# Kernel tuning notes

Measured on AMD Instinct MI355X. Metric: run time of the kernel, lower is better.

## Reference

```python
import jax, jax.numpy as jnp
import numpy as np

N = 100000   # nodes
E = 1600000  # directed edges
NF = 128     # n_feat
NH = 128     # n_hid
NC = 64      # n_class


def _glorot(key, fan_in, fan_out):
    lim = (6.0 / (fan_in + fan_out)) ** 0.5
    return jax.random.uniform(key, (fan_in, fan_out), dtype=jnp.float32, minval=-lim, maxval=lim)


def setup_inputs() -> dict:
    key = jax.random.key(0)
    ks = jax.random.split(key, 10)
    x = jax.random.normal(ks[0], (N, NF), dtype=jnp.float32)
    edge_index = jax.random.randint(ks[1], (2, E), 0, N, dtype=jnp.int32)
    return {
        "x": x,
        "edge_index": edge_index,
        "W_in": _glorot(ks[2], NF, NH),
        "b_in": jnp.zeros((NH,), jnp.float32),
        "W_mid0": _glorot(ks[3], NH, NH),
        "b_mid0": jnp.zeros((NH,), jnp.float32),
        "W_mid1": _glorot(ks[4], NH, NH),
        "b_mid1": jnp.zeros((NH,), jnp.float32),
        "W_out": _glorot(ks[5], NH, NC),
        "b_out": jnp.zeros((NC,), jnp.float32),
        "W_skip_out": _glorot(ks[6], NH, NC),
    }


def _gcn_conv(x, W, b, src, dst, coef, n):
    # x' = D^-1/2 (A + I) D^-1/2 (x W) + b   (symmetric-normalized GCN conv)
    h = x @ W                               # [N, out]
    msg = h[src] * coef[:, None]            # [E+N, out] gather + scale
    return jax.ops.segment_sum(msg, dst, num_segments=n) + b


def reference(x, edge_index, W_in, b_in, W_mid0, b_mid0, W_mid1, b_mid1, W_out, b_out, W_skip_out):
    loops = jnp.arange(N, dtype=edge_index.dtype)
    src = jnp.concatenate([edge_index[0], loops])  # add self-loops
    dst = jnp.concatenate([edge_index[1], loops])
    deg = jax.ops.segment_sum(jnp.ones_like(dst, dtype=jnp.float32), dst, num_segments=N)
    dinv = jax.lax.rsqrt(deg)                      # deg >= 1 due to self-loops
    coef = dinv[src] * dinv[dst]                   # [E+N]

    # in layer: conv + res skip (NF == NH so plain add) + relu; dropout is no-op in eval
    h = _gcn_conv(x, W_in, b_in, src, dst, coef, N)
    x = jax.nn.relu(h + x)
    # mid layers
    for W, b in ((W_mid0, b_mid0), (W_mid1, b_mid1)):
        h = _gcn_conv(x, W, b, src, dst, coef, N)
        x = jax.nn.relu(h + x)
    # out layer: conv + res skip with channel projection NH -> NC
    h = _gcn_conv(x, W_out, b_out, src, dst, coef, N)
    return h + x @ W_skip_out
```

## Files before the change

kernel.cpp:

```cpp
#include <hip/hip_runtime.h>
#include <hip/hip_bf16.h>

constexpr int NN = 100000;
constexpr int NE = 1600000;
constexpr int NH = 128;
constexpr int NC = 64;
constexpr int BKN  = 256;
constexpr int NB2  = (NN + BKN - 1) / BKN;
constexpr int TILE = 4096;
constexpr int NT   = (NE + TILE - 1) / TILE;

__device__ __forceinline__ unsigned short f2bf(float f) {
    unsigned int u = __float_as_uint(f);
    unsigned int r = (u + 0x7fffu + ((u >> 16) & 1u)) >> 16;
    return (unsigned short)r;
}
__device__ __forceinline__ float bflo(unsigned int u) { return __uint_as_float(u << 16); }
__device__ __forceinline__ float bfhi(unsigned int u) { return __uint_as_float(u & 0xffff0000u); }
__device__ __forceinline__ float bf2f(unsigned short h) { return __uint_as_float(((unsigned int)h) << 16); }
__device__ __forceinline__ unsigned int pack2bf(float lo, float hi) {
    return (unsigned int)f2bf(lo) | ((unsigned int)f2bf(hi) << 16);
}

typedef __bf16 v8bf __attribute__((ext_vector_type(8)));
typedef float  v4f  __attribute__((ext_vector_type(4)));

constexpr size_t OFF_BCNT  = 0;
constexpr size_t OFF_BBASE = OFF_BCNT  + 2048;
constexpr size_t OFF_BCUR  = OFF_BBASE + 2048;
constexpr size_t OFF_RP    = OFF_BCUR  + 2048;
constexpr size_t OFF_DINV  = OFF_RP    + 400384;
constexpr size_t OFF_COL   = OFF_DINV  + 400384;
constexpr size_t OFF_WT    = OFF_COL   + 6400000;
constexpr size_t OFF_H     = OFF_WT    + 32768;
constexpr size_t OFF_X     = OFF_H     + 25600000;


__global__ __launch_bounds__(256) void bhist_kernel(const int* __restrict__ edst,
                                                    int* __restrict__ bcnt) {
    __shared__ int h[NB2];
    for (int i = threadIdx.x; i < NB2; i += 256) h[i] = 0;
    __syncthreads();
    const int base = blockIdx.x * TILE;
    #pragma unroll
    for (int j = 0; j < 16; ++j) {
        int e = base + j * 256 + threadIdx.x;
        if (e < NE) atomicAdd(&h[edst[e] >> 8], 1);
    }
    __syncthreads();
    for (int i = threadIdx.x; i < NB2; i += 256)
        if (h[i]) atomicAdd(&bcnt[i], h[i]);
}

__global__ __launch_bounds__(512) void bscan_kernel(const int* __restrict__ bcnt,
                                                    int* __restrict__ bbase,
                                                    int* __restrict__ bcur) {
    __shared__ int s[512];
    const int t = threadIdx.x;
    int v = (t < NB2) ? bcnt[t] : 0;
    s[t] = v;
    __syncthreads();
    for (int off = 1; off < 512; off <<= 1) {
        int a = (t >= off) ? s[t - off] : 0;
        __syncthreads();
        s[t] += a;
        __syncthreads();
    }
    int excl = s[t] - v;
    if (t < NB2) { bbase[t] = excl; bcur[t] = excl; }
    if (t == NB2 - 1) bbase[NB2] = excl + v;
}

__global__ __launch_bounds__(256) void scatter2_kernel(const int* __restrict__ esrc,
                                                       const int* __restrict__ edst,
                                                       int* __restrict__ bcur,
                                                       int2* __restrict__ ebuf) {
    __shared__ int h[NB2];
    __shared__ int cur[NB2];
    for (int i = threadIdx.x; i < NB2; i += 256) h[i] = 0;
    __syncthreads();
    const int base = blockIdx.x * TILE;
    #pragma unroll
    for (int j = 0; j < 16; ++j) {
        int e = base + j * 256 + threadIdx.x;
        if (e < NE) atomicAdd(&h[edst[e] >> 8], 1);
    }
    __syncthreads();
    for (int i = threadIdx.x; i < NB2; i += 256) {
        int c = h[i];
        cur[i] = c ? atomicAdd(&bcur[i], c) : 0;
    }
    __syncthreads();
    #pragma unroll
    for (int j = 0; j < 16; ++j) {
        int e = base + j * 256 + threadIdx.x;
        if (e < NE) {
            int s = esrc[e], d = edst[e];
            int pos = atomicAdd(&cur[d >> 8], 1);
            ebuf[pos] = make_int2(s, d);
        }
    }
}

__global__ __launch_bounds__(256) void csrfill2_kernel(const int2* __restrict__ ebuf,
                                                       const int* __restrict__ bbase,
                                                       int* __restrict__ rp,
                                                       float* __restrict__ dinv,
                                                       int* __restrict__ col) {
    __shared__ int cnt[256];
    __shared__ int cursor[256];
    __shared__ int s[256];
    __shared__ int sbeg, send;
    const int b = blockIdx.x;
    const int t = threadIdx.x;
    if (t == 0) { sbeg = bbase[b]; send = bbase[b + 1]; }
    cnt[t] = 0;
    __syncthreads();
    const int beg = sbeg, end = send;
    const int node0 = b * BKN;

    for (int e = beg + t; e < end; e += 256)
        atomicAdd(&cnt[ebuf[e].y & 255], 1);
    __syncthreads();

    int v = cnt[t];
    s[t] = v;
    __syncthreads();
    for (int off = 1; off < 256; off <<= 1) {
        int a = (t >= off) ? s[t - off] : 0;
        __syncthreads();
        s[t] += a;
        __syncthreads();
    }
    int excl = s[t] - v;
    int gnode = node0 + t;
    if (gnode < NN) {
        rp[gnode]   = beg + excl;
        dinv[gnode] = rsqrtf((float)(v + 1));
    }
    cursor[t] = beg + excl;
    if (b == NB2 - 1 && t == 0) rp[NN] = NE;
    __syncthreads();

    for (int e = beg + t; e < end; e += 256) {
        int2 sd = ebuf[e];
        int pos = atomicAdd(&cursor[sd.y & 255], 1);
        col[pos] = sd.x;
    }
}

__global__ __launch_bounds__(256) void wpre_kernel(const float* __restrict__ W0,
                                                   const float* __restrict__ W1,
                                                   int wstride,
                                                   unsigned short* __restrict__ Wt) {
    int e = blockIdx.x * 256 + threadIdx.x;
    int k = e >> 7, c = e & 127;
    float v = (c < 64) ? W0[(size_t)k * wstride + c] : W1[(size_t)k * wstride + (c - 64)];
    Wt[c * 128 + k] = f2bf(v);
}

constexpr int XROW = 136;

template<bool XF32>
__global__ __launch_bounds__(256) void gemm_mfma_kernel(const void* __restrict__ Xv,
                                                        const unsigned short* __restrict__ Wt,
                                                        const float* __restrict__ dinv,
                                                        int scaleMask,
                                                        unsigned short* __restrict__ Hb) {
    __shared__ unsigned short Wl[128 * XROW];
    __shared__ unsigned short Xl[64 * XROW];

    const int t = threadIdx.x;
    const int rowBase = blockIdx.x * 64;

    #pragma unroll
    for (int i = 0; i < 8; ++i) {
        int f = i * 256 + t;
        int r = f >> 4, c8 = f & 15;
        uint4 w = *(const uint4*)&Wt[r * 128 + c8 * 8];
        *(uint4*)&Wl[r * XROW + c8 * 8] = w;
    }
    if (XF32) {
        const float* X = (const float*)Xv;
        #pragma unroll
        for (int i = 0; i < 8; ++i) {
            int f = i * 256 + t;
            int r = f >> 5, c4 = f & 31;
            int gn = rowBase + r;
            float4 v = make_float4(0.f, 0.f, 0.f, 0.f);
            if (gn < NN) v = *(const float4*)&X[(size_t)gn * 128 + c4 * 4];
            ushort4 o;
            o.x = f2bf(v.x); o.y = f2bf(v.y); o.z = f2bf(v.z); o.w = f2bf(v.w);
            *(ushort4*)&Xl[r * XROW + c4 * 4] = o;
        }
    } else {
        const unsigned short* X = (const unsigned short*)Xv;
        #pragma unroll
        for (int i = 0; i < 4; ++i) {
            int f = i * 256 + t;
            int r = f >> 4, c8 = f & 15;
            int gn = rowBase + r;
            uint4 v = make_uint4(0u, 0u, 0u, 0u);
            if (gn < NN) v = *(const uint4*)&X[(size_t)gn * 128 + c8 * 8];
            *(uint4*)&Xl[r * XROW + c8 * 8] = v;
        }
    }
    __syncthreads();

    const int w  = t >> 6;
    const int l  = t & 63;
    const int lr = l & 15;
    const int lk = (l >> 4) * 8;

    v4f acc[8];
    #pragma unroll
    for (int n = 0; n < 8; ++n) acc[n] = (v4f){0.f, 0.f, 0.f, 0.f};

    const unsigned short* ax = &Xl[(w * 16 + lr) * XROW + lk];
    const unsigned short* bx = &Wl[lr * XROW + lk];

    #pragma unroll
    for (int kk = 0; kk < 4; ++kk) {
        v8bf a = *(const v8bf*)&ax[kk * 32];
        #pragma unroll
        for (int n = 0; n < 8; ++n) {
            v8bf b = *(const v8bf*)&bx[(n * 16) * XROW + kk * 32];
            acc[n] = __builtin_amdgcn_mfma_f32_16x16x32_bf16(a, b, acc[n], 0, 0, 0);
        }
    }

    #pragma unroll
    for (int r_ = 0; r_ < 4; ++r_) {
        int row  = w * 16 + (l >> 4) * 4 + r_;
        int grow = rowBase + row;
        float dsc = dinv[grow < NN ? grow : NN - 1];
        #pragma unroll
        for (int n = 0; n < 8; ++n) {
            float sc = ((scaleMask >> (n >> 2)) & 1) ? dsc : 1.f;
            Xl[row * XROW + n * 16 + lr] = f2bf(acc[n][r_] * sc);
        }
    }
    __syncthreads();

    #pragma unroll
    for (int i = 0; i < 4; ++i) {
        int f = i * 256 + t;
        int r = f >> 4, c8 = f & 15;
        int gn = rowBase + r;
        if (gn < NN) {
            uint4 v = *(const uint4*)&Xl[r * XROW + c8 * 8];
            *(uint4*)&Hb[(size_t)gn * 128 + c8 * 8] = v;
        }
    }
}

template<bool XF32>
__global__ __launch_bounds__(256) void agg128_kernel(const unsigned short* __restrict__ Hb,
                                                     const void* __restrict__ Xoldv,
                                                     const int* __restrict__ rp,
                                                     const int* __restrict__ col,
                                                     const float* __restrict__ dinv,
                                                     const float* __restrict__ bias,
                                                     unsigned int* __restrict__ Xnew) {
    const int wid  = threadIdx.x >> 6;
    const int lane = threadIdx.x & 63;
    const int i = blockIdx.x * 4 + wid;
    if (i >= NN) return;

    const unsigned int* __restrict__ Hu = (const unsigned int*)Hb;

    const float di = dinv[i];
    const float2 b2 = ((const float2*)bias)[lane];
    float xox, xoy;
    if (XF32) {
        float2 xo = ((const float2*)Xoldv)[(size_t)i * 64 + lane];
        xox = xo.x; xoy = xo.y;
    } else {
        unsigned int xo = ((const unsigned int*)Xoldv)[(size_t)i * 64 + lane];
        xox = bflo(xo); xoy = bfhi(xo);
    }

    unsigned int us = Hu[(size_t)i * 64 + lane];
    float ax = bflo(us), ay = bfhi(us);

    const int beg = rp[i], end = rp[i + 1];
    int e = beg;
    for (; e + 8 <= end; e += 8) {
        int s0 = col[e],     s1 = col[e + 1], s2 = col[e + 2], s3 = col[e + 3];
        int s4 = col[e + 4], s5 = col[e + 5], s6 = col[e + 6], s7 = col[e + 7];
        unsigned int u0 = Hu[(size_t)s0 * 64 + lane];
        unsigned int u1 = Hu[(size_t)s1 * 64 + lane];
        unsigned int u2 = Hu[(size_t)s2 * 64 + lane];
        unsigned int u3 = Hu[(size_t)s3 * 64 + lane];
        unsigned int u4 = Hu[(size_t)s4 * 64 + lane];
        unsigned int u5 = Hu[(size_t)s5 * 64 + lane];
        unsigned int u6 = Hu[(size_t)s6 * 64 + lane];
        unsigned int u7 = Hu[(size_t)s7 * 64 + lane];
        ax += ((bflo(u0) + bflo(u1)) + (bflo(u2) + bflo(u3))) +
              ((bflo(u4) + bflo(u5)) + (bflo(u6) + bflo(u7)));
        ay += ((bfhi(u0) + bfhi(u1)) + (bfhi(u2) + bfhi(u3))) +
              ((bfhi(u4) + bfhi(u5)) + (bfhi(u6) + bfhi(u7)));
    }
    for (; e + 4 <= end; e += 4) {
        int s0 = col[e], s1 = col[e + 1], s2 = col[e + 2], s3 = col[e + 3];
        unsigned int u0 = Hu[(size_t)s0 * 64 + lane];
        unsigned int u1 = Hu[(size_t)s1 * 64 + lane];
        unsigned int u2 = Hu[(size_t)s2 * 64 + lane];
        unsigned int u3 = Hu[(size_t)s3 * 64 + lane];
        ax += (bflo(u0) + bflo(u1)) + (bflo(u2) + bflo(u3));
        ay += (bfhi(u0) + bfhi(u1)) + (bfhi(u2) + bfhi(u3));
    }
    for (; e < end; ++e) {
        unsigned int u = Hu[(size_t)col[e] * 64 + lane];
        ax += bflo(u);
        ay += bfhi(u);
    }

    float ox = fmaxf(di * ax + b2.x + xox, 0.f);
    float oy = fmaxf(di * ay + b2.y + xoy, 0.f);
    Xnew[(size_t)i * 64 + lane] = pack2bf(ox, oy);
}

__global__ __launch_bounds__(256) void aggout_kernel(const unsigned short* __restrict__ Hb,
                                                     const int* __restrict__ rp,
                                                     const int* __restrict__ col,
                                                     const float* __restrict__ dinv,
                                                     const float* __restrict__ bias,
                                                     float* __restrict__ out) {
    const int wid  = threadIdx.x >> 6;
    const int lane = threadIdx.x & 63;
    const int i = blockIdx.x * 4 + wid;
    if (i >= NN) return;

    const float di = dinv[i];
    const float b  = bias[lane];
    const float sk = bf2f(Hb[(size_t)i * 128 + 64 + lane]);

    float a = bf2f(Hb[(size_t)i * 128 + lane]);
    const int beg = rp[i], end = rp[i + 1];
    int e = beg;
    for (; e + 8 <= end; e += 8) {
        int s0 = col[e],     s1 = col[e + 1], s2 = col[e + 2], s3 = col[e + 3];
        int s4 = col[e + 4], s5 = col[e + 5], s6 = col[e + 6], s7 = col[e + 7];
        float m0 = bf2f(Hb[(size_t)s0 * 128 + lane]);
        float m1 = bf2f(Hb[(size_t)s1 * 128 + lane]);
        float m2 = bf2f(Hb[(size_t)s2 * 128 + lane]);
        float m3 = bf2f(Hb[(size_t)s3 * 128 + lane]);
        float m4 = bf2f(Hb[(size_t)s4 * 128 + lane]);
        float m5 = bf2f(Hb[(size_t)s5 * 128 + lane]);
        float m6 = bf2f(Hb[(size_t)s6 * 128 + lane]);
        float m7 = bf2f(Hb[(size_t)s7 * 128 + lane]);
        a += ((m0 + m1) + (m2 + m3)) + ((m4 + m5) + (m6 + m7));
    }
    for (; e + 4 <= end; e += 4) {
        int s0 = col[e], s1 = col[e + 1], s2 = col[e + 2], s3 = col[e + 3];
        float m0 = bf2f(Hb[(size_t)s0 * 128 + lane]);
        float m1 = bf2f(Hb[(size_t)s1 * 128 + lane]);
        float m2 = bf2f(Hb[(size_t)s2 * 128 + lane]);
        float m3 = bf2f(Hb[(size_t)s3 * 128 + lane]);
        a += (m0 + m1) + (m2 + m3);
    }
    for (; e < end; ++e) a += bf2f(Hb[(size_t)col[e] * 128 + lane]);

    out[(size_t)i * 64 + lane] = di * a + b + sk;
}

extern "C" void kernel_launch(void* const* d_in, const int* in_sizes, int n_in,
                              void* d_out, int out_size, void* d_ws, size_t ws_size,
                              hipStream_t stream) {
    const float* x      = (const float*)d_in[0];
    const int*   ei     = (const int*)d_in[1];
    const float* W_in   = (const float*)d_in[2];
    const float* b_in   = (const float*)d_in[3];
    const float* W_mid0 = (const float*)d_in[4];
    const float* b_mid0 = (const float*)d_in[5];
    const float* W_mid1 = (const float*)d_in[6];
    const float* b_mid1 = (const float*)d_in[7];
    const float* W_out  = (const float*)d_in[8];
    const float* b_out  = (const float*)d_in[9];
    const float* W_skip = (const float*)d_in[10];

    const int* esrc = ei;
    const int* edst = ei + NE;

    char* ws = (char*)d_ws;
    int*   bcnt   = (int*)  (ws + OFF_BCNT);
    int*   bbase  = (int*)  (ws + OFF_BBASE);
    int*   bcur   = (int*)  (ws + OFF_BCUR);
    int*   rp     = (int*)  (ws + OFF_RP);
    float* dinv   = (float*)(ws + OFF_DINV);
    int*   col    = (int*)  (ws + OFF_COL);
    unsigned short* wt   = (unsigned short*)(ws + OFF_WT);
    unsigned short* hbuf = (unsigned short*)(ws + OFF_H);
    int2*  ebuf   = (int2*) (ws + OFF_H);
    unsigned short* xbuf = (unsigned short*)(ws + OFF_X);
    unsigned int*   xbufw = (unsigned int*)(ws + OFF_X);
    float* outp   = (float*)d_out;

    const int gemmGrid = (NN + 63) / 64;
    const int aggGrid  = (NN + 3) / 4;

    hipMemsetAsync(bcnt, 0, (size_t)(NB2 + 1) * 4, stream);
    bhist_kernel<<<NT, 256, 0, stream>>>(edst, bcnt);
    bscan_kernel<<<1, 512, 0, stream>>>(bcnt, bbase, bcur);
    scatter2_kernel<<<NT, 256, 0, stream>>>(esrc, edst, bcur, ebuf);
    csrfill2_kernel<<<NB2, 256, 0, stream>>>(ebuf, bbase, rp, dinv, col);

    wpre_kernel<<<64, 256, 0, stream>>>(W_in, W_in + 64, 128, wt);
    gemm_mfma_kernel<true><<<gemmGrid, 256, 0, stream>>>(x, wt, dinv, 3, hbuf);
    agg128_kernel<true><<<aggGrid, 256, 0, stream>>>(hbuf, x, rp, col, dinv, b_in, xbufw);

    wpre_kernel<<<64, 256, 0, stream>>>(W_mid0, W_mid0 + 64, 128, wt);
    gemm_mfma_kernel<false><<<gemmGrid, 256, 0, stream>>>(xbuf, wt, dinv, 3, hbuf);
    agg128_kernel<false><<<aggGrid, 256, 0, stream>>>(hbuf, xbuf, rp, col, dinv, b_mid0, xbufw);

    wpre_kernel<<<64, 256, 0, stream>>>(W_mid1, W_mid1 + 64, 128, wt);
    gemm_mfma_kernel<false><<<gemmGrid, 256, 0, stream>>>(xbuf, wt, dinv, 3, hbuf);
    agg128_kernel<false><<<aggGrid, 256, 0, stream>>>(hbuf, xbuf, rp, col, dinv, b_mid1, xbufw);

    wpre_kernel<<<64, 256, 0, stream>>>(W_out, W_skip, 64, wt);
    gemm_mfma_kernel<false><<<gemmGrid, 256, 0, stream>>>(xbuf, wt, dinv, 1, hbuf);
    aggout_kernel<<<aggGrid, 256, 0, stream>>>(hbuf, rp, col, dinv, b_out, outp);
}
```

Before: 385.9 us.

## Store hidden-layer gather features as FP8 and pack edge buffer into 32-bit words

The GEMM for the first three layers now writes the dinv-scaled hidden features as FP8 (e4m3) instead of bf16, and the aggregation kernels gather 2-byte FP8 pairs and convert them with the hardware packed converter. This halves the bytes fetched per neighbour in the random-gather aggregation, which is meant to be memory-bound. Separately, the CSR build packs source id and low destination byte into one 32-bit word instead of an int2, halving the temporary edge buffer traffic. The cost is a large precision loss in the hidden features, which may break accuracy tolerances. The packing also assumes node ids fit in 24 bits.

```diff
diff --git a/kernel.cpp b/kernel.cpp
--- a/kernel.cpp
+++ b/kernel.cpp
@@ -3,8 +3,6 @@
 
 constexpr int NN = 100000;
 constexpr int NE = 1600000;
-constexpr int NH = 128;
-constexpr int NC = 64;
 constexpr int BKN  = 256;
 constexpr int NB2  = (NN + BKN - 1) / BKN;
 constexpr int TILE = 4096;
@@ -24,6 +22,11 @@
 
 typedef __bf16 v8bf __attribute__((ext_vector_type(8)));
 typedef float  v4f  __attribute__((ext_vector_type(4)));
+typedef float  v2f  __attribute__((ext_vector_type(2)));
+
+__device__ __forceinline__ v2f fp8x2_to_f32(unsigned int u) {
+    return __builtin_amdgcn_cvt_pk_f32_fp8(u, false);
+}
 
 constexpr size_t OFF_BCNT  = 0;
 constexpr size_t OFF_BBASE = OFF_BCNT  + 2048;
@@ -32,7 +35,8 @@
 constexpr size_t OFF_DINV  = OFF_RP    + 400384;
 constexpr size_t OFF_COL   = OFF_DINV  + 400384;
 constexpr size_t OFF_WT    = OFF_COL   + 6400000;
-constexpr size_t OFF_H     = OFF_WT    + 32768;
+constexpr size_t OFF_H8    = OFF_WT    + 32768;
+constexpr size_t OFF_H     = OFF_H8    + 12800000;
 constexpr size_t OFF_X     = OFF_H     + 25600000;
 
 
@@ -74,7 +78,7 @@
 __global__ __launch_bounds__(256) void scatter2_kernel(const int* __restrict__ esrc,
                                                        const int* __restrict__ edst,
                                                        int* __restrict__ bcur,
-                                                       int2* __restrict__ ebuf) {
+                                                       unsigned int* __restrict__ ebuf) {
     __shared__ int h[NB2];
     __shared__ int cur[NB2];
     for (int i = threadIdx.x; i < NB2; i += 256) h[i] = 0;
@@ -97,12 +101,12 @@
         if (e < NE) {
             int s = esrc[e], d = edst[e];
             int pos = atomicAdd(&cur[d >> 8], 1);
-            ebuf[pos] = make_int2(s, d);
-        }
-    }
-}
-
-__global__ __launch_bounds__(256) void csrfill2_kernel(const int2* __restrict__ ebuf,
+            ebuf[pos] = (unsigned int)s | ((unsigned int)(d & 255) << 24);
+        }
+    }
+}
+
+__global__ __launch_bounds__(256) void csrfill2_kernel(const unsigned int* __restrict__ ebuf,
                                                        const int* __restrict__ bbase,
                                                        int* __restrict__ rp,
                                                        float* __restrict__ dinv,
@@ -120,7 +124,7 @@
     const int node0 = b * BKN;
 
     for (int e = beg + t; e < end; e += 256)
-        atomicAdd(&cnt[ebuf[e].y & 255], 1);
+        atomicAdd(&cnt[ebuf[e] >> 24], 1);
     __syncthreads();
 
     int v = cnt[t];
@@ -143,9 +147,9 @@
     __syncthreads();
 
     for (int e = beg + t; e < end; e += 256) {
-        int2 sd = ebuf[e];
-        int pos = atomicAdd(&cursor[sd.y & 255], 1);
-        col[pos] = sd.x;
+        unsigned int sd = ebuf[e];
+        int pos = atomicAdd(&cursor[sd >> 24], 1);
+        col[pos] = (int)(sd & 0xFFFFFFu);
     }
 }
 
@@ -161,12 +165,12 @@
 
 constexpr int XROW = 136;
 
-template<bool XF32>
+template<bool XF32, bool OUT8>
 __global__ __launch_bounds__(256) void gemm_mfma_kernel(const void* __restrict__ Xv,
                                                         const unsigned short* __restrict__ Wt,
                                                         const float* __restrict__ dinv,
                                                         int scaleMask,
-                                                        unsigned short* __restrict__ Hb) {
+                                                        void* __restrict__ Ho) {
     __shared__ unsigned short Wl[128 * XROW];
     __shared__ unsigned short Xl[64 * XROW];
 
@@ -242,20 +246,39 @@
     }
     __syncthreads();
 
-    #pragma unroll
-    for (int i = 0; i < 4; ++i) {
-        int f = i * 256 + t;
-        int r = f >> 4, c8 = f & 15;
-        int gn = rowBase + r;
-        if (gn < NN) {
-            uint4 v = *(const uint4*)&Xl[r * XROW + c8 * 8];
-            *(uint4*)&Hb[(size_t)gn * 128 + c8 * 8] = v;
+    if (OUT8) {
+        unsigned char* H8 = (unsigned char*)Ho;
+        #pragma unroll
+        for (int i = 0; i < 4; ++i) {
+            int f = i * 256 + t;
+            int r = f >> 4, c8 = f & 15;
+            int gn = rowBase + r;
+            if (gn < NN) {
+                uint4 v = *(const uint4*)&Xl[r * XROW + c8 * 8];
+                unsigned int lo = __builtin_amdgcn_cvt_pk_fp8_f32(bflo(v.x), bfhi(v.x), 0u, false);
+                lo = __builtin_amdgcn_cvt_pk_fp8_f32(bflo(v.y), bfhi(v.y), lo, true);
+                unsigned int hi = __builtin_amdgcn_cvt_pk_fp8_f32(bflo(v.z), bfhi(v.z), 0u, false);
+                hi = __builtin_amdgcn_cvt_pk_fp8_f32(bflo(v.w), bfhi(v.w), hi, true);
+                *(uint2*)&H8[(size_t)gn * 128 + c8 * 8] = make_uint2(lo, hi);
+            }
+        }
+    } else {
+        unsigned short* Hb = (unsigned short*)Ho;
+        #pragma unroll
+        for (int i = 0; i < 4; ++i) {
+            int f = i * 256 + t;
+            int r = f >> 4, c8 = f & 15;
+            int gn = rowBase + r;
+            if (gn < NN) {
+                uint4 v = *(const uint4*)&Xl[r * XROW + c8 * 8];
+                *(uint4*)&Hb[(size_t)gn * 128 + c8 * 8] = v;
+            }
         }
     }
 }
 
 template<bool XF32>
-__global__ __launch_bounds__(256) void agg128_kernel(const unsigned short* __restrict__ Hb,
+__global__ __launch_bounds__(256) void agg128_kernel(const unsigned char* __restrict__ H8,
                                                      const void* __restrict__ Xoldv,
                                                      const int* __restrict__ rp,
                                                      const int* __restrict__ col,
@@ -267,7 +290,7 @@
     const int i = blockIdx.x * 4 + wid;
     if (i >= NN) return;
 
-    const unsigned int* __restrict__ Hu = (const unsigned int*)Hb;
+    const unsigned short* __restrict__ Hs = (const unsigned short*)H8;
 
     const float di = dinv[i];
     const float2 b2 = ((const float2*)bias)[lane];
@@ -280,40 +303,44 @@
         xox = bflo(xo); xoy = bfhi(xo);
     }
 
-    unsigned int us = Hu[(size_t)i * 64 + lane];
-    float ax = bflo(us), ay = bfhi(us);
+    v2f sf = fp8x2_to_f32(Hs[(size_t)i * 64 + lane]);
+    float ax = sf.x, ay = sf.y;
 
     const int beg = rp[i], end = rp[i + 1];
     int e = beg;
     for (; e + 8 <= end; e += 8) {
         int s0 = col[e],     s1 = col[e + 1], s2 = col[e + 2], s3 = col[e + 3];
         int s4 = col[e + 4], s5 = col[e + 5], s6 = col[e + 6], s7 = col[e + 7];
-        unsigned int u0 = Hu[(size_t)s0 * 64 + lane];
-        unsigned int u1 = Hu[(size_t)s1 * 64 + lane];
-        unsigned int u2 = Hu[(size_t)s2 * 64 + lane];
-        unsigned int u3 = Hu[(size_t)s3 * 64 + lane];
-        unsigned int u4 = Hu[(size_t)s4 * 64 + lane];
-        unsigned int u5 = Hu[(size_t)s5 * 64 + lane];
-        unsigned int u6 = Hu[(size_t)s6 * 64 + lane];
-        unsigned int u7 = Hu[(size_t)s7 * 64 + lane];
-        ax += ((bflo(u0) + bflo(u1)) + (bflo(u2) + bflo(u3))) +
-              ((bflo(u4) + bflo(u5)) + (bflo(u6) + bflo(u7)));
-        ay += ((bfhi(u0) + bfhi(u1)) + (bfhi(u2) + bfhi(u3))) +
-              ((bfhi(u4) + bfhi(u5)) + (bfhi(u6) + bfhi(u7)));
+        unsigned int u0 = Hs[(size_t)s0 * 64 + lane];
+        unsigned int u1 = Hs[(size_t)s1 * 64 + lane];
+        unsigned int u2 = Hs[(size_t)s2 * 64 + lane];
+        unsigned int u3 = Hs[(size_t)s3 * 64 + lane];
+        unsigned int u4 = Hs[(size_t)s4 * 64 + lane];
+        unsigned int u5 = Hs[(size_t)s5 * 64 + lane];
+        unsigned int u6 = Hs[(size_t)s6 * 64 + lane];
+        unsigned int u7 = Hs[(size_t)s7 * 64 + lane];
+        v2f m0 = fp8x2_to_f32(u0), m1 = fp8x2_to_f32(u1);
+        v2f m2 = fp8x2_to_f32(u2), m3 = fp8x2_to_f32(u3);
+        v2f m4 = fp8x2_to_f32(u4), m5 = fp8x2_to_f32(u5);
+        v2f m6 = fp8x2_to_f32(u6), m7 = fp8x2_to_f32(u7);
+        ax += ((m0.x + m1.x) + (m2.x + m3.x)) + ((m4.x + m5.x) + (m6.x + m7.x));
+        ay += ((m0.y + m1.y) + (m2.y + m3.y)) + ((m4.y + m5.y) + (m6.y + m7.y));
     }
     for (; e + 4 <= end; e += 4) {
         int s0 = col[e], s1 = col[e + 1], s2 = col[e + 2], s3 = col[e + 3];
-        unsigned int u0 = Hu[(size_t)s0 * 64 + lane];
-        unsigned int u1 = Hu[(size_t)s1 * 64 + lane];
-        unsigned int u2 = Hu[(size_t)s2 * 64 + lane];
-        unsigned int u3 = Hu[(size_t)s3 * 64 + lane];
-        ax += (bflo(u0) + bflo(u1)) + (bflo(u2) + bflo(u3));
-        ay += (bfhi(u0) + bfhi(u1)) + (bfhi(u2) + bfhi(u3));
+        unsigned int u0 = Hs[(size_t)s0 * 64 + lane];
+        unsigned int u1 = Hs[(size_t)s1 * 64 + lane];
+        unsigned int u2 = Hs[(size_t)s2 * 64 + lane];
+        unsigned int u3 = Hs[(size_t)s3 * 64 + lane];
+        v2f m0 = fp8x2_to_f32(u0), m1 = fp8x2_to_f32(u1);
+        v2f m2 = fp8x2_to_f32(u2), m3 = fp8x2_to_f32(u3);
+        ax += (m0.x + m1.x) + (m2.x + m3.x);
+        ay += (m0.y + m1.y) + (m2.y + m3.y);
     }
     for (; e < end; ++e) {
-        unsigned int u = Hu[(size_t)col[e] * 64 + lane];
-        ax += bflo(u);
-        ay += bfhi(u);
+        v2f m = fp8x2_to_f32(Hs[(size_t)col[e] * 64 + lane]);
+        ax += m.x;
+        ay += m.y;
     }
 
     float ox = fmaxf(di * ax + b2.x + xox, 0.f);
@@ -391,10 +418,11 @@
     float* dinv   = (float*)(ws + OFF_DINV);
     int*   col    = (int*)  (ws + OFF_COL);
     unsigned short* wt   = (unsigned short*)(ws + OFF_WT);
+    unsigned char*  h8   = (unsigned char*) (ws + OFF_H8);
     unsigned short* hbuf = (unsigned short*)(ws + OFF_H);
-    int2*  ebuf   = (int2*) (ws + OFF_H);
+    unsigned int*   ebuf = (unsigned int*)  (ws + OFF_H);
     unsigned short* xbuf = (unsigned short*)(ws + OFF_X);
-    unsigned int*   xbufw = (unsigned int*)(ws + OFF_X);
+    unsigned int*   xbufw = (unsigned int*) (ws + OFF_X);
     float* outp   = (float*)d_out;
 
     const int gemmGrid = (NN + 63) / 64;
@@ -407,18 +435,18 @@
     csrfill2_kernel<<<NB2, 256, 0, stream>>>(ebuf, bbase, rp, dinv, col);
 
     wpre_kernel<<<64, 256, 0, stream>>>(W_in, W_in + 64, 128, wt);
-    gemm_mfma_kernel<true><<<gemmGrid, 256, 0, stream>>>(x, wt, dinv, 3, hbuf);
-    agg128_kernel<true><<<aggGrid, 256, 0, stream>>>(hbuf, x, rp, col, dinv, b_in, xbufw);
+    gemm_mfma_kernel<true, true><<<gemmGrid, 256, 0, stream>>>(x, wt, dinv, 3, h8);
+    agg128_kernel<true><<<aggGrid, 256, 0, stream>>>(h8, x, rp, col, dinv, b_in, xbufw);
 
     wpre_kernel<<<64, 256, 0, stream>>>(W_mid0, W_mid0 + 64, 128, wt);
-    gemm_mfma_kernel<false><<<gemmGrid, 256, 0, stream>>>(xbuf, wt, dinv, 3, hbuf);
-    agg128_kernel<false><<<aggGrid, 256, 0, stream>>>(hbuf, xbuf, rp, col, dinv, b_mid0, xbufw);
+    gemm_mfma_kernel<false, true><<<gemmGrid, 256, 0, stream>>>(xbuf, wt, dinv, 3, h8);
+    agg128_kernel<false><<<aggGrid, 256, 0, stream>>>(h8, xbuf, rp, col, dinv, b_mid0, xbufw);
 
     wpre_kernel<<<64, 256, 0, stream>>>(W_mid1, W_mid1 + 64, 128, wt);
-    gemm_mfma_kernel<false><<<gemmGrid, 256, 0, stream>>>(xbuf, wt, dinv, 3, hbuf);
-    agg128_kernel<false><<<aggGrid, 256, 0, stream>>>(hbuf, xbuf, rp, col, dinv, b_mid1, xbufw);
+    gemm_mfma_kernel<false, true><<<gemmGrid, 256, 0, stream>>>(xbuf, wt, dinv, 3, h8);
+    agg128_kernel<false><<<aggGrid, 256, 0, stream>>>(h8, xbuf, rp, col, dinv, b_mid1, xbufw);
 
     wpre_kernel<<<64, 256, 0, stream>>>(W_out, W_skip, 64, wt);
-    gemm_mfma_kernel<false><<<gemmGrid, 256, 0, stream>>>(xbuf, wt, dinv, 1, hbuf);
+    gemm_mfma_kernel<false, false><<<gemmGrid, 256, 0, stream>>>(xbuf, wt, dinv, 1, hbuf);
     aggout_kernel<<<aggGrid, 256, 0, stream>>>(hbuf, rp, col, dinv, b_out, outp);
 }
```

After: 339.5 us. 1.14x faster.
